# Performance work log

Hardware: AMD Instinct MI355X
Metric: run time of the kernel (lower is better)

The kernel has to match this reference:

```python
import jax, jax.numpy as jnp
import numpy as np

HID = 64   # RNN_HID_SIZE
FEAT = 9   # feature dim, hard-coded in module
T = 36     # SEQ_LEN


def setup_inputs() -> dict:
    key = jax.random.key(0)
    ks = jax.random.split(key, 20)
    B = 16384

    def u(k, shape, stdv):
        return jax.random.uniform(k, shape, jnp.float32, -stdv, stdv)

    s_h = 1.0 / np.sqrt(HID)    # stdv for layers with 64 rows / fan-in 64
    s_f = 1.0 / np.sqrt(FEAT)   # stdv 1/3 for feature-sized layers
    s_c = 1.0 / np.sqrt(2 * FEAT)  # weight_combine: Linear(18, 9)

    inp = {
        "values": jax.random.normal(ks[0], (B, T, FEAT), jnp.float32),
        "masks": (jax.random.uniform(ks[1], (B, T, FEAT)) < 0.8).astype(jnp.float32),
        "deltas": jax.random.uniform(ks[2], (B, T, FEAT), jnp.float32, 0.0, 5.0),
        # TemporalDecay h: W [64, 9], stdv = 1/sqrt(64)
        "W_gh": u(ks[3], (HID, FEAT), s_h), "b_gh": u(ks[4], (HID,), s_h),
        # TemporalDecay x (diag): W [9, 9], stdv = 1/sqrt(9)
        "W_gx": u(ks[5], (FEAT, FEAT), s_f), "b_gx": u(ks[6], (FEAT,), s_f),
        # hist_reg: Linear(64, 9)
        "W_hist": u(ks[7], (FEAT, HID), s_h), "b_hist": u(ks[8], (FEAT,), s_h),
        "W_feat": u(ks[9], (FEAT, FEAT), s_f), "b_feat": u(ks[10], (FEAT,), s_f),
        # weight_combine: Linear(18, 9)
        "W_comb": u(ks[11], (FEAT, 2 * FEAT), s_c), "b_comb": u(ks[12], (FEAT,), s_c),
        # LSTMCell(18, 64): gates order i, f, g, o
        "W_ih": u(ks[13], (4 * HID, 2 * FEAT), s_h), "W_hh": u(ks[14], (4 * HID, HID), s_h),
        "b_ih": u(ks[15], (4 * HID,), s_h), "b_hh": u(ks[16], (4 * HID,), s_h),
    }
    return inp


def reference(values, masks, deltas, W_gh, b_gh, W_gx, b_gx, W_hist, b_hist,
              W_feat, b_feat, W_comb, b_comb, W_ih, W_hh, b_ih, b_hh):
    B = values.shape[0]
    dt = values.dtype
    eye = jnp.eye(FEAT, dtype=dt)
    Wgx_diag = W_gx * eye            # TemporalDecay diag mask
    Wfeat_off = W_feat * (1.0 - eye)

    # time-major for scan: [T, B, F]
    xs = (jnp.swapaxes(values, 0, 1), jnp.swapaxes(masks, 0, 1), jnp.swapaxes(deltas, 0, 1))

    def step(carry, xt):
        h, c, loss = carry
        x, m, d = xt
        gamma_h = jnp.exp(-jax.nn.relu(d @ W_gh.T + b_gh))   # [B, 64]
        gamma_x = jnp.exp(-jax.nn.relu(d @ Wgx_diag.T + b_gx))  # [B, 9]
        h = h * gamma_h
        x_h = h @ W_hist.T + b_hist
        denom = jnp.sum(m) + 1e-5
        x_c = m * x + (1.0 - m) * x_h
        z_h = x_c @ Wfeat_off.T + b_feat
        alpha = jnp.concatenate([gamma_x, m], axis=1) @ W_comb.T + b_comb
        c_h = alpha * z_h + (1.0 - alpha) * x_h
        loss = loss + (jnp.sum(jnp.abs(x - x_h) * m)
                       + jnp.sum(jnp.abs(x - z_h) * m)
                       + jnp.sum(jnp.abs(x - c_h) * m)) / denom
        c_c = m * x + (1.0 - m) * c_h
        inp = jnp.concatenate([c_c, m], axis=1)              # [B, 18]
        gates = inp @ W_ih.T + b_ih + h @ W_hh.T + b_hh      # [B, 256]
        i, f, g, o = jnp.split(gates, 4, axis=1)
        c = jax.nn.sigmoid(f) * c + jax.nn.sigmoid(i) * jnp.tanh(g)
        h = jax.nn.sigmoid(o) * jnp.tanh(c)
        return (h, c, loss), c_c

    init = (jnp.zeros((B, HID), dt), jnp.zeros((B, HID), dt), jnp.zeros((), dt))
    (_, _, loss), imps = jax.lax.scan(step, init, xs)
    imputations = jnp.swapaxes(imps, 0, 1)  # [B, T, F]
    return loss / T, imputations
```

## Files before the change

kernel.cpp:

```cpp
#include <hip/hip_runtime.h>

typedef _Float16 hh;
typedef _Float16 h2  __attribute__((ext_vector_type(2)));
typedef _Float16 v4h __attribute__((ext_vector_type(4)));
typedef _Float16 v8h __attribute__((ext_vector_type(8)));
typedef float v4f    __attribute__((ext_vector_type(4)));
typedef unsigned short u16;

#define T_STEPS 36
#define FEAT 9
#define HID 64
#define BT 32
#define SIN_STR 232
#define PK_STR 40

__device__ __forceinline__ float fast_exp2(float x) {
#if __has_builtin(__builtin_amdgcn_exp2f)
  return __builtin_amdgcn_exp2f(x);
#else
  return exp2f(x);
#endif
}
__device__ __forceinline__ float fast_rcp(float x) {
#if __has_builtin(__builtin_amdgcn_rcpf)
  return __builtin_amdgcn_rcpf(x);
#else
  return 1.f / x;
#endif
}
__device__ __forceinline__ float sigmoid_fast(float x) {
  return fast_rcp(1.f + fast_exp2(x * -1.442695041f));
}
__device__ __forceinline__ float tanh_fast(float x) {
  return 1.f - 2.f * fast_rcp(1.f + fast_exp2(x * 2.885390082f));
}
__device__ __forceinline__ float fdot2(h2 a, h2 b, float c) {
#if __has_builtin(__builtin_amdgcn_fdot2)
  return __builtin_amdgcn_fdot2(a, b, c, false);
#else
  return c + (float)a[0] * (float)b[0] + (float)a[1] * (float)b[1];
#endif
}
__device__ __forceinline__ h2 mkh2(hh a, hh b) { h2 r; r[0] = a; r[1] = b; return r; }
__device__ __forceinline__ v4f mfma16(v8h a, v8h b, v4f c) {
  return __builtin_amdgcn_mfma_f32_16x16x32_f16(a, b, c, 0, 0, 0);
}

__global__ void zero_ws(float* __restrict__ ws, float* __restrict__ out) {
  int tid = threadIdx.x;
  if (tid < T_STEPS) ws[tid] = 0.f;
  if (tid == 0) out[0] = 0.f;
}

__global__ __launch_bounds__(256) void denom_kernel(const float* __restrict__ masks,
                                                    float* __restrict__ ws) {
  __shared__ float red[T_STEPS];
  const int tid = threadIdx.x;
  if (tid < T_STEPS) red[tid] = 0.f;
  __syncthreads();
  const int idx = blockIdx.x * 256 + tid;
  const int t0 = (idx % 9) * 4;
  const float4* p = (const float4*)masks + (size_t)idx * 9;
  float acc[4] = {0.f, 0.f, 0.f, 0.f};
#pragma unroll
  for (int c = 0; c < 9; ++c) {
    float4 v = p[c];
    acc[(4 * c) / 9]     += v.x;
    acc[(4 * c + 1) / 9] += v.y;
    acc[(4 * c + 2) / 9] += v.z;
    acc[(4 * c + 3) / 9] += v.w;
  }
#pragma unroll
  for (int j = 0; j < 4; ++j) atomicAdd(&red[t0 + j], acc[j]);
  __syncthreads();
  if (tid < T_STEPS) atomicAdd(&ws[tid], red[tid]);
}

#define BARX() asm volatile("s_waitcnt lgkmcnt(0)\n\ts_barrier" ::: "memory")

#define RITS_STEP(t, pxC,pmC,pdC,pxCb,pmCb,pdCb, pxN,pmN,pdN,pxNb,pmNb,pdNb)   \
  {                                                                            \
    const float inv_den = fast_rcp(denom[(t)] + 1e-5f);                        \
    const int pb = ((t) & 1) * 96;                                             \
         \
    v4f gacc[2];                                                               \
    {                                                                          \
      const int sel = ((t) + 1) & 1;                                           \
      const int awin = 176 + sel * 24;                                         \
      _Pragma("unroll")                                                        \
      for (int mt = 0; mt < 2; ++mt) {                                         \
        v8h a_ = *(const v8h*)&sIn[(mt * 16 + nlo) * SIN_STR + awin + q * 8];  \
        v4f z4 = {0.f, 0.f, 0.f, 0.f};                                         \
        gacc[mt] = sel ? mfma16(a_, bGamB, z4) : mfma16(a_, bGamA, z4);        \
      }                                                                        \
    }                                                                          \
       \
    {                                                                          \
      v4f xacc = {0.f, 0.f, 0.f, 0.f};                                         \
      _Pragma("unroll")                                                        \
      for (int kt = 0; kt < 3; ++kt) {                                         \
        v8h a_ = *(const v8h*)&sIn[(mtw * 16 + nlo) * SIN_STR + pb +           \
                                   kt * 32 + q * 8];                           \
        xacc = mfma16(a_, bH[kt], xacc);                                       \
      }                                                                        \
         \
      if ((q >> 1) == (wid & 1) && nlo < 9) {                                  \
        _Pragma("unroll")                                                      \
        for (int r = 0; r < 4; ++r)                                            \
          sPk[(mtw * 16 + q * 4 + r) * PK_STR + 18 + nlo] = (hh)xacc[r];       \
      }                                                                        \
    }                                                                          \
           \
    asm volatile("s_waitcnt lgkmcnt(0)" ::: "memory");                         \
                 \
    {                                                                          \
      const int pk = eP * PK_STR;                                              \
      float x_f  = (float)sPk[pk + fqw];                                       \
      float m_f  = (float)sPk[pk + 9 + fqw];                                   \
      float xh_f = (float)sPk[pk + 18 + fqw];                                  \
      v8h r0 = *(const v8h*)&sPk[pk];                                          \
      v8h r1 = *(const v8h*)&sPk[pk + 8];                                      \
      v8h r2 = *(const v8h*)&sPk[pk + 16];                                     \
      v8h r3 = *(const v8h*)&sPk[pk + 24];                                     \
      v4h r4 = *(const v4h*)&sPk[pk + 32];                                     \
      hh xxh[9] = {r0[0],r0[1],r0[2],r0[3],r0[4],r0[5],r0[6],r0[7],r1[0]};     \
      hh mmh[9] = {r1[1],r1[2],r1[3],r1[4],r1[5],r1[6],r1[7],r2[0],r2[1]};     \
      hh xhh[9] = {r2[2],r2[3],r2[4],r2[5],r2[6],r2[7],r3[0],r3[1],r3[2]};     \
      hh gxh[9] = {r3[3],r3[4],r3[5],r3[6],r3[7],r4[0],r4[1],r4[2],r4[3]};     \
      hh xch[10];                                                              \
      _Pragma("unroll")                                                        \
      for (int f = 0; f < 9; ++f) {                                            \
        u16 mb = __builtin_bit_cast(u16, mmh[f]);                              \
        xch[f] = mb ? xxh[f] : xhh[f];                                         \
      }                                                                        \
      xch[9] = (hh)0.f;                                                        \
      h2 xc2[5] = {mkh2(xch[0],xch[1]), mkh2(xch[2],xch[3]),                   \
                   mkh2(xch[4],xch[5]), mkh2(xch[6],xch[7]),                   \
                   mkh2(xch[8],xch[9])};                                       \
      h2 g2[9]  = {mkh2(gxh[0],gxh[1]), mkh2(gxh[2],gxh[3]),                   \
                   mkh2(gxh[4],gxh[5]), mkh2(gxh[6],gxh[7]),                   \
                   mkh2(gxh[8],mmh[0]), mkh2(mmh[1],mmh[2]),                   \
                   mkh2(mmh[3],mmh[4]), mkh2(mmh[5],mmh[6]),                   \
                   mkh2(mmh[7],mmh[8])};                                       \
                        \
      float z1a = bf1, z1b = 0.f;                                              \
      z1a = fdot2(wf1[0], xc2[0], z1a); z1b = fdot2(wf1[1], xc2[1], z1b);      \
      z1a = fdot2(wf1[2], xc2[2], z1a); z1b = fdot2(wf1[3], xc2[3], z1b);      \
      z1a = fdot2(wf1[4], xc2[4], z1a);                                        \
      float z1 = z1a + z1b;                                                    \
      float a1a = bc1v, a1b = 0.f, a1c = 0.f;                                  \
      a1a = fdot2(wc1[0], g2[0], a1a); a1b = fdot2(wc1[1], g2[1], a1b);        \
      a1c = fdot2(wc1[2], g2[2], a1c); a1a = fdot2(wc1[3], g2[3], a1a);        \
      a1b = fdot2(wc1[4], g2[4], a1b); a1c = fdot2(wc1[5], g2[5], a1c);        \
      a1a = fdot2(wc1[6], g2[6], a1a); a1b = fdot2(wc1[7], g2[7], a1b);        \
      a1c = fdot2(wc1[8], g2[8], a1c);                                         \
      float a1 = (a1a + a1b) + a1c;                                            \
      float ch1 = xh_f + a1 * (z1 - xh_f);                                     \
      bool obs1 = (m_f != 0.f);                                                \
      float cc1 = obs1 ? x_f : ch1;                                            \
      float lterm = obs1 ? (fabsf(x_f - xh_f) + fabsf(x_f - z1) +              \
                            fabsf(x_f - ch1)) : 0.f;                           \
      sIn[eP * SIN_STR + pb + fqw] = (hh)cc1;                                  \
      sIn[eP * SIN_STR + pb + 9 + fqw] = (hh)m_f;                              \
      out[1 + (size_t)(b0 + eP) * (T_STEPS * FEAT) + (t) * FEAT + fqw] = cc1;  \
      if (fqw == 7) {                                                          \
        float z2a = bf2, z2b = 0.f;                                            \
        z2a = fdot2(wf2[0], xc2[0], z2a); z2b = fdot2(wf2[1], xc2[1], z2b);    \
        z2a = fdot2(wf2[2], xc2[2], z2a); z2b = fdot2(wf2[3], xc2[3], z2b);    \
        z2a = fdot2(wf2[4], xc2[4], z2a);                                      \
        float z2 = z2a + z2b;                                                  \
        float a2a = bc2v, a2b = 0.f, a2c = 0.f;                                \
        a2a = fdot2(wc2[0], g2[0], a2a); a2b = fdot2(wc2[1], g2[1], a2b);      \
        a2c = fdot2(wc2[2], g2[2], a2c); a2a = fdot2(wc2[3], g2[3], a2a);      \
        a2b = fdot2(wc2[4], g2[4], a2b); a2c = fdot2(wc2[5], g2[5], a2c);      \
        a2a = fdot2(wc2[6], g2[6], a2a); a2b = fdot2(wc2[7], g2[7], a2b);      \
        a2c = fdot2(wc2[8], g2[8], a2c);                                       \
        float a2 = (a2a + a2b) + a2c;                                          \
        float x8 = (float)xxh[8], m8 = (float)mmh[8], xh8 = (float)xhh[8];     \
        float ch2 = xh8 + a2 * (z2 - xh8);                                     \
        bool obs2 = (m8 != 0.f);                                               \
        float cc2 = obs2 ? x8 : ch2;                                           \
        lterm += obs2 ? (fabsf(x8 - xh8) + fabsf(x8 - z2) +                    \
                         fabsf(x8 - ch2)) : 0.f;                               \
        sIn[eP * SIN_STR + pb + 8] = (hh)cc2;                                  \
        sIn[eP * SIN_STR + pb + 17] = mmh[8];                                  \
        out[1 + (size_t)(b0 + eP) * (T_STEPS * FEAT) + (t) * FEAT + 8] = cc2;  \
      }                                                                        \
      loss_acc += lterm * inv_den;                                             \
    }                                                                          \
    BARX();                                                                    \
      \
    {                                                                          \
      const bool ldN = ((t) + 2 < T_STEPS);                                    \
      const bool ldD = ((t) + 3 < T_STEPS);                                    \
      if (ldN) {                                                               \
        size_t offn = (size_t)(b0 + e1) * (T_STEPS * FEAT) +                   \
                      ((t) + 2) * FEAT + f1;                                   \
        pxN = values[offn]; pmN = masks[offn];                                 \
        if (tid < 32) {                                                        \
          size_t offn2 = (size_t)(b0 + e2g) * (T_STEPS * FEAT) +               \
                         ((t) + 2) * FEAT + f2g;                               \
          pxNb = values[offn2]; pmNb = masks[offn2];                           \
        }                                                                      \
      }                                                                        \
      if (ldD) {                                                               \
        size_t offd = (size_t)(b0 + e1) * (T_STEPS * FEAT) +                   \
                      ((t) + 3) * FEAT + f1;                                   \
        pdN = deltas[offd];                                                    \
        if (tid < 32) {                                                        \
          size_t offd2 = (size_t)(b0 + e2g) * (T_STEPS * FEAT) +               \
                         ((t) + 3) * FEAT + f2g;                               \
          pdNb = deltas[offd2];                                                \
        }                                                                      \
      }                                                                        \
      const int pub = (((t) + 1) & 1) * 96;                                    \
      v8h af[2][3];                                                            \
      _Pragma("unroll")                                                        \
      for (int mt = 0; mt < 2; ++mt)                                           \
        _Pragma("unroll")                                                      \
        for (int kt = 0; kt < 3; ++kt)                                         \
          af[mt][kt] = *(const v8h*)&sIn[(mt * 16 + nlo) * SIN_STR + pb +      \
                                         kt * 32 + q * 8];                     \
      v4f acc[2][4];                                                           \
      _Pragma("unroll")                                                        \
      for (int mt = 0; mt < 2; ++mt)                                           \
        _Pragma("unroll")                                                      \
        for (int p = 0; p < 4; ++p)                                            \
          acc[mt][p] = (v4f){0.f, 0.f, 0.f, 0.f};                              \
      _Pragma("unroll")                                                        \
      for (int mt = 0; mt < 2; ++mt)                                           \
        _Pragma("unroll")                                                      \
        for (int p = 0; p < 4; ++p)                                            \
          _Pragma("unroll")                                                    \
          for (int kt = 0; kt < 3; ++kt)                                       \
            acc[mt][p] = mfma16(af[mt][kt], bG[p][kt], acc[mt][p]);            \
      _Pragma("unroll")                                                        \
      for (int mt = 0; mt < 2; ++mt) {                                         \
        _Pragma("unroll")                                                      \
        for (int r = 0; r < 4; ++r) {                                          \
          float ig = sigmoid_fast(acc[mt][0][r]);                              \
          float fg = sigmoid_fast(acc[mt][1][r]);                              \
          float gg = tanh_fast(acc[mt][2][r]);                                 \
          float og = sigmoid_fast(acc[mt][3][r]);                              \
          float cn = fg * c_s[mt * 4 + r] + ig * gg;                           \
          c_s[mt * 4 + r] = cn;                                                \
          float hn = og * tanh_fast(cn);                                       \
          float gam = fast_exp2(fmaxf(gacc[mt][r], 0.f) * -1.442695041f);      \
          sIn[(mt * 16 + q * 4 + r) * SIN_STR + pub + 18 + j_col] =            \
              (hh)(hn * gam);                                                  \
        }                                                                      \
      }                                                                        \
      if ((t) + 1 < T_STEPS) {                                                 \
        sPk[e1 * PK_STR + f1] = (hh)pxC;                                       \
        sPk[e1 * PK_STR + 9 + f1] = (hh)pmC;                                   \
        sPk[e1 * PK_STR + 27 + f1] =                                           \
            (hh)fast_exp2(fmaxf(dH * wgx1 + bgx1, 0.f) * -1.442695041f);       \
        if (tid < 32) {                                                        \
          sPk[e2g * PK_STR + f2g] = (hh)pxCb;                                  \
          sPk[e2g * PK_STR + 9 + f2g] = (hh)pmCb;                              \
          sPk[e2g * PK_STR + 27 + f2g] =                                       \
              (hh)fast_exp2(fmaxf(dHb * wgx2 + bgx2, 0.f) * -1.442695041f);    \
        }                                                                      \
      }                                                                        \
      if ((t) + 2 < T_STEPS) {                                                 \
        const int sb = 192 + ((t) & 1) * 10;                                   \
        sIn[e1 * SIN_STR + sb + f1] = (hh)pdC;                                 \
        if (tid < 32) sIn[e2g * SIN_STR + sb + f2g] = (hh)pdCb;                \
      }                                                                        \
      dH = pdC; dHb = pdCb;                                                    \
    }                                                                          \
    BARX();                                                                    \
  }

__global__ __launch_bounds__(256, 2) void rits_kernel(
    const float* __restrict__ values, const float* __restrict__ masks,
    const float* __restrict__ deltas,
    const float* __restrict__ W_gh, const float* __restrict__ b_gh,
    const float* __restrict__ W_gx, const float* __restrict__ b_gx,
    const float* __restrict__ W_hist, const float* __restrict__ b_hist,
    const float* __restrict__ W_feat, const float* __restrict__ b_feat,
    const float* __restrict__ W_comb, const float* __restrict__ b_comb,
    const float* __restrict__ W_ih, const float* __restrict__ W_hh,
    const float* __restrict__ b_ih, const float* __restrict__ b_hh,
    const float* __restrict__ denom, float* __restrict__ out) {

  __shared__ __align__(16) hh sIn[BT * SIN_STR];
  __shared__ __align__(16) hh sPk[BT * PK_STR];
  __shared__ float sRed[256];

  const int tid = threadIdx.x;
  const int lane = tid & 63;
  const int wid = tid >> 6;
  const int q = lane >> 4;
  const int nlo = lane & 15;
  const int b0 = blockIdx.x * BT;
  const int j_col = 16 * wid + nlo;
  const int mtw = wid >> 1;

  v8h bG[4][3];
#pragma unroll
  for (int p = 0; p < 4; ++p)
#pragma unroll
    for (int kt = 0; kt < 3; ++kt) {
      int n = 64 * p + j_col;
      v8h r;
#pragma unroll
      for (int jj = 0; jj < 8; ++jj) {
        int k = kt * 32 + q * 8 + jj;
        float v = 0.f;
        if (k < 18)       v = W_ih[n * 18 + k];
        else if (k < 82)  v = W_hh[n * 64 + (k - 18)];
        else if (k == 82) v = b_ih[n] + b_hh[n];
        r[jj] = (hh)v;
      }
      bG[p][kt] = r;
    }
  v8h bH[3];
#pragma unroll
  for (int kt = 0; kt < 3; ++kt) {
    v8h r;
#pragma unroll
    for (int jj = 0; jj < 8; ++jj) {
      int k = kt * 32 + q * 8 + jj;
      float v = 0.f;
      if (nlo < 9) {
        if (k >= 18 && k < 82) v = W_hist[nlo * 64 + (k - 18)];
        else if (k == 82)      v = b_hist[nlo];
      }
      r[jj] = (hh)v;
    }
    bH[kt] = r;
  }
  v8h bGamA, bGamB;
  {
    int n = j_col;
    v8h ra, rb;
#pragma unroll
    for (int jj = 0; jj < 8; ++jj) {
      int k = q * 8 + jj;
      float va = 0.f, vb = 0.f;
      if (k == 2) va = b_gh[n];
      else if (k >= 16 && k < 25) va = W_gh[n * 9 + (k - 16)];
      if (k >= 2 && k < 11) vb = W_gh[n * 9 + (k - 2)];
      else if (k == 12) vb = b_gh[n];
      ra[jj] = (hh)va; rb[jj] = (hh)vb;
    }
    bGamA = ra; bGamB = rb;
  }

  const int eP = tid >> 3, fqw = tid & 7;
  h2 wf1[5], wf2[5], wc1[9], wc2[9];
  float bf1 = b_feat[fqw], bf2 = b_feat[8];
  float bc1v = b_comb[fqw], bc2v = b_comb[8];
#pragma unroll
  for (int j = 0; j < 5; ++j) {
    int i0 = 2 * j, i1 = 2 * j + 1;
    hh a0 = (hh)((i0 == fqw) ? 0.f : W_feat[fqw * 9 + i0]);
    hh a1 = (hh)((i1 < 9) ? ((i1 == fqw) ? 0.f : W_feat[fqw * 9 + i1]) : 0.f);
    wf1[j] = mkh2(a0, a1);
    hh c0 = (hh)((i0 == 8) ? 0.f : W_feat[8 * 9 + i0]);
    hh c1 = (hh)((i1 < 9) ? W_feat[8 * 9 + i1] : 0.f);
    wf2[j] = mkh2(c0, c1);
  }
#pragma unroll
  for (int j = 0; j < 9; ++j) {
    wc1[j] = mkh2((hh)W_comb[fqw * 18 + 2 * j], (hh)W_comb[fqw * 18 + 2 * j + 1]);
    wc2[j] = mkh2((hh)W_comb[8 * 18 + 2 * j], (hh)W_comb[8 * 18 + 2 * j + 1]);
  }

  const int e1 = tid / 9, f1 = tid - 9 * e1;
  const int e2g = (tid + 256) / 9, f2g = (tid + 256) - 9 * e2g;
  const float wgx1 = W_gx[f1 * 9 + f1], bgx1 = b_gx[f1];
  float wgx2 = 0.f, bgx2 = 0.f;
  if (tid < 32) { wgx2 = W_gx[f2g * 9 + f2g]; bgx2 = b_gx[f2g]; }

  for (int i = tid; i < BT * SIN_STR; i += 256) sIn[i] = (hh)0.f;
  __syncthreads();
  if (tid < BT) {
    sIn[tid * SIN_STR + 82] = (hh)1.f;
    sIn[tid * SIN_STR + 178] = (hh)1.f;
    sIn[tid * SIN_STR + 212] = (hh)1.f;
  }
  float pA_x = 0.f, pA_m = 0.f, pA_d = 0.f, pA_xb = 0.f, pA_mb = 0.f, pA_db = 0.f;
  float pB_x = 0.f, pB_m = 0.f, pB_d = 0.f, pB_xb = 0.f, pB_mb = 0.f, pB_db = 0.f;
  float dH = 0.f, dHb = 0.f;
  {
    size_t off = (size_t)(b0 + e1) * (T_STEPS * FEAT) + f1;
    float d0 = deltas[off];
    sPk[e1 * PK_STR + f1] = (hh)values[off];
    sPk[e1 * PK_STR + 9 + f1] = (hh)masks[off];
    sPk[e1 * PK_STR + 27 + f1] =
        (hh)fast_exp2(fmaxf(d0 * wgx1 + bgx1, 0.f) * -1.442695041f);
    float d1 = deltas[off + FEAT];
    dH = d1;
    sIn[e1 * SIN_STR + 202 + f1] = (hh)d1;
    pA_x = values[off + FEAT]; pA_m = masks[off + FEAT];
    pA_d = deltas[off + 2 * FEAT];
    if (tid < 32) {
      size_t off2 = (size_t)(b0 + e2g) * (T_STEPS * FEAT) + f2g;
      float d0b = deltas[off2];
      sPk[e2g * PK_STR + f2g] = (hh)values[off2];
      sPk[e2g * PK_STR + 9 + f2g] = (hh)masks[off2];
      sPk[e2g * PK_STR + 27 + f2g] =
          (hh)fast_exp2(fmaxf(d0b * wgx2 + bgx2, 0.f) * -1.442695041f);
      float d1b = deltas[off2 + FEAT];
      dHb = d1b;
      sIn[e2g * SIN_STR + 202 + f2g] = (hh)d1b;
      pA_xb = values[off2 + FEAT]; pA_mb = masks[off2 + FEAT];
      pA_db = deltas[off2 + 2 * FEAT];
    }
  }
  __syncthreads();

  float c_s[8];
#pragma unroll
  for (int i = 0; i < 8; ++i) c_s[i] = 0.f;
  float loss_acc = 0.f;

  for (int t = 0; t < T_STEPS; t += 2) {
    RITS_STEP(t,     pA_x, pA_m, pA_d, pA_xb, pA_mb, pA_db,
                     pB_x, pB_m, pB_d, pB_xb, pB_mb, pB_db);
    RITS_STEP(t + 1, pB_x, pB_m, pB_d, pB_xb, pB_mb, pB_db,
                     pA_x, pA_m, pA_d, pA_xb, pA_mb, pA_db);
  }

  sRed[tid] = loss_acc;
  __syncthreads();
  for (int k = 128; k > 0; k >>= 1) {
    if (tid < k) sRed[tid] += sRed[tid + k];
    __syncthreads();
  }
  if (tid == 0) atomicAdd(out, sRed[0] * (1.f / (float)T_STEPS));
}

extern "C" void kernel_launch(void* const* d_in, const int* in_sizes, int n_in,
                              void* d_out, int out_size, void* d_ws, size_t ws_size,
                              hipStream_t stream) {
  const float* values = (const float*)d_in[0];
  const float* masks  = (const float*)d_in[1];
  const float* deltas = (const float*)d_in[2];
  const float* W_gh   = (const float*)d_in[3];
  const float* b_gh   = (const float*)d_in[4];
  const float* W_gx   = (const float*)d_in[5];
  const float* b_gx   = (const float*)d_in[6];
  const float* W_hist = (const float*)d_in[7];
  const float* b_hist = (const float*)d_in[8];
  const float* W_feat = (const float*)d_in[9];
  const float* b_feat = (const float*)d_in[10];
  const float* W_comb = (const float*)d_in[11];
  const float* b_comb = (const float*)d_in[12];
  const float* W_ih   = (const float*)d_in[13];
  const float* W_hh   = (const float*)d_in[14];
  const float* b_ih   = (const float*)d_in[15];
  const float* b_hh   = (const float*)d_in[16];

  float* out = (float*)d_out;
  float* ws  = (float*)d_ws;
  int B = in_sizes[0] / (T_STEPS * FEAT);

  zero_ws<<<1, 64, 0, stream>>>(ws, out);
  denom_kernel<<<(B * 9) / 256, 256, 0, stream>>>(masks, ws);
  rits_kernel<<<B / BT, 256, 0, stream>>>(values, masks, deltas,
                                          W_gh, b_gh, W_gx, b_gx,
                                          W_hist, b_hist, W_feat, b_feat,
                                          W_comb, b_comb, W_ih, W_hh,
                                          b_ih, b_hh, ws, out);
}
```

Measured before the change: 245.4 us.

## Interleave two independent batch tiles per block to halve barriers per step

Each block now processes two 32-row batch tiles in lockstep, with separate shared buffers, cell states and prefetch registers per tile. The phases of both tiles are interleaved inside one step, so each pair of barriers covers twice the work and the independent instruction streams can hide each other's latency. The grid halves and launch bounds drop to one block per SM-equivalent, trading occupancy and register headroom for more instruction-level parallelism within a block.

```diff
diff --git a/kernel.cpp b/kernel.cpp
--- a/kernel.cpp
+++ b/kernel.cpp
@@ -11,6 +11,7 @@
 #define FEAT 9
 #define HID 64
 #define BT 32
+#define NT 2
 #define SIN_STR 232
 #define PK_STR 40
 
@@ -78,51 +79,48 @@
 
 #define BARX() asm volatile("s_waitcnt lgkmcnt(0)\n\ts_barrier" ::: "memory")
 
-#define RITS_STEP(t, pxC,pmC,pdC,pxCb,pmCb,pdCb, pxN,pmN,pdN,pxNb,pmNb,pdNb)   \
+
+#define TILE_GXH(t, TI)                                                        \
   {                                                                            \
-    const float inv_den = fast_rcp(denom[(t)] + 1e-5f);                        \
     const int pb = ((t) & 1) * 96;                                             \
-         \
-    v4f gacc[2];                                                               \
     {                                                                          \
       const int sel = ((t) + 1) & 1;                                           \
       const int awin = 176 + sel * 24;                                         \
       _Pragma("unroll")                                                        \
       for (int mt = 0; mt < 2; ++mt) {                                         \
-        v8h a_ = *(const v8h*)&sIn[(mt * 16 + nlo) * SIN_STR + awin + q * 8];  \
+        v8h a_ = *(const v8h*)&sIn##TI[(mt * 16 + nlo) * SIN_STR + awin + q * 8]; \
         v4f z4 = {0.f, 0.f, 0.f, 0.f};                                         \
-        gacc[mt] = sel ? mfma16(a_, bGamB, z4) : mfma16(a_, bGamA, z4);        \
+        gacc##TI[mt] = sel ? mfma16(a_, bGamB, z4) : mfma16(a_, bGamA, z4);    \
       }                                                                        \
     }                                                                          \
-       \
     {                                                                          \
       v4f xacc = {0.f, 0.f, 0.f, 0.f};                                         \
       _Pragma("unroll")                                                        \
       for (int kt = 0; kt < 3; ++kt) {                                         \
-        v8h a_ = *(const v8h*)&sIn[(mtw * 16 + nlo) * SIN_STR + pb +           \
-                                   kt * 32 + q * 8];                           \
+        v8h a_ = *(const v8h*)&sIn##TI[(mtw * 16 + nlo) * SIN_STR + pb +       \
+                                       kt * 32 + q * 8];                       \
         xacc = mfma16(a_, bH[kt], xacc);                                       \
       }                                                                        \
-         \
       if ((q >> 1) == (wid & 1) && nlo < 9) {                                  \
         _Pragma("unroll")                                                      \
         for (int r = 0; r < 4; ++r)                                            \
-          sPk[(mtw * 16 + q * 4 + r) * PK_STR + 18 + nlo] = (hh)xacc[r];       \
+          sPk##TI[(mtw * 16 + q * 4 + r) * PK_STR + 18 + nlo] = (hh)xacc[r];   \
       }                                                                        \
     }                                                                          \
-           \
-    asm volatile("s_waitcnt lgkmcnt(0)" ::: "memory");                         \
-                 \
+  }
+
+#define TILE_P2(t, TI)                                                         \
     {                                                                          \
+      const int pb = ((t) & 1) * 96;                                           \
       const int pk = eP * PK_STR;                                              \
-      float x_f  = (float)sPk[pk + fqw];                                       \
-      float m_f  = (float)sPk[pk + 9 + fqw];                                   \
-      float xh_f = (float)sPk[pk + 18 + fqw];                                  \
-      v8h r0 = *(const v8h*)&sPk[pk];                                          \
-      v8h r1 = *(const v8h*)&sPk[pk + 8];                                      \
-      v8h r2 = *(const v8h*)&sPk[pk + 16];                                     \
-      v8h r3 = *(const v8h*)&sPk[pk + 24];                                     \
-      v4h r4 = *(const v4h*)&sPk[pk + 32];                                     \
+      float x_f  = (float)sPk##TI[pk + fqw];                                   \
+      float m_f  = (float)sPk##TI[pk + 9 + fqw];                               \
+      float xh_f = (float)sPk##TI[pk + 18 + fqw];                              \
+      v8h r0 = *(const v8h*)&sPk##TI[pk];                                      \
+      v8h r1 = *(const v8h*)&sPk##TI[pk + 8];                                  \
+      v8h r2 = *(const v8h*)&sPk##TI[pk + 16];                                 \
+      v8h r3 = *(const v8h*)&sPk##TI[pk + 24];                                 \
+      v4h r4 = *(const v4h*)&sPk##TI[pk + 32];                                 \
       hh xxh[9] = {r0[0],r0[1],r0[2],r0[3],r0[4],r0[5],r0[6],r0[7],r1[0]};     \
       hh mmh[9] = {r1[1],r1[2],r1[3],r1[4],r1[5],r1[6],r1[7],r2[0],r2[1]};     \
       hh xhh[9] = {r2[2],r2[3],r2[4],r2[5],r2[6],r2[7],r3[0],r3[1],r3[2]};     \
@@ -142,7 +140,6 @@
                    mkh2(gxh[8],mmh[0]), mkh2(mmh[1],mmh[2]),                   \
                    mkh2(mmh[3],mmh[4]), mkh2(mmh[5],mmh[6]),                   \
                    mkh2(mmh[7],mmh[8])};                                       \
-                        \
       float z1a = bf1, z1b = 0.f;                                              \
       z1a = fdot2(wf1[0], xc2[0], z1a); z1b = fdot2(wf1[1], xc2[1], z1b);      \
       z1a = fdot2(wf1[2], xc2[2], z1a); z1b = fdot2(wf1[3], xc2[3], z1b);      \
@@ -160,9 +157,10 @@
       float cc1 = obs1 ? x_f : ch1;                                            \
       float lterm = obs1 ? (fabsf(x_f - xh_f) + fabsf(x_f - z1) +              \
                             fabsf(x_f - ch1)) : 0.f;                           \
-      sIn[eP * SIN_STR + pb + fqw] = (hh)cc1;                                  \
-      sIn[eP * SIN_STR + pb + 9 + fqw] = (hh)m_f;                              \
-      out[1 + (size_t)(b0 + eP) * (T_STEPS * FEAT) + (t) * FEAT + fqw] = cc1;  \
+      sIn##TI[eP * SIN_STR + pb + fqw] = (hh)cc1;                              \
+      sIn##TI[eP * SIN_STR + pb + 9 + fqw] = (hh)m_f;                          \
+      out[1 + (size_t)(b0T##TI + eP) * (T_STEPS * FEAT) + (t) * FEAT + fqw] =  \
+          cc1;                                                                 \
       if (fqw == 7) {                                                          \
         float z2a = bf2, z2b = 0.f;                                            \
         z2a = fdot2(wf2[0], xc2[0], z2a); z2b = fdot2(wf2[1], xc2[1], z2b);    \
@@ -182,45 +180,47 @@
         float cc2 = obs2 ? x8 : ch2;                                           \
         lterm += obs2 ? (fabsf(x8 - xh8) + fabsf(x8 - z2) +                    \
                          fabsf(x8 - ch2)) : 0.f;                               \
-        sIn[eP * SIN_STR + pb + 8] = (hh)cc2;                                  \
-        sIn[eP * SIN_STR + pb + 17] = mmh[8];                                  \
-        out[1 + (size_t)(b0 + eP) * (T_STEPS * FEAT) + (t) * FEAT + 8] = cc2;  \
+        sIn##TI[eP * SIN_STR + pb + 8] = (hh)cc2;                              \
+        sIn##TI[eP * SIN_STR + pb + 17] = mmh[8];                              \
+        out[1 + (size_t)(b0T##TI + eP) * (T_STEPS * FEAT) + (t) * FEAT + 8] =  \
+            cc2;                                                               \
       }                                                                        \
       loss_acc += lterm * inv_den;                                             \
-    }                                                                          \
-    BARX();                                                                    \
-      \
+    }
+
+#define TILE_B(t, TI, CUR, NXT)                                                \
     {                                                                          \
       const bool ldN = ((t) + 2 < T_STEPS);                                    \
       const bool ldD = ((t) + 3 < T_STEPS);                                    \
       if (ldN) {                                                               \
-        size_t offn = (size_t)(b0 + e1) * (T_STEPS * FEAT) +                   \
+        size_t offn = (size_t)(b0T##TI + e1) * (T_STEPS * FEAT) +              \
                       ((t) + 2) * FEAT + f1;                                   \
-        pxN = values[offn]; pmN = masks[offn];                                 \
+        p##TI##NXT##_x = values[offn]; p##TI##NXT##_m = masks[offn];           \
         if (tid < 32) {                                                        \
-          size_t offn2 = (size_t)(b0 + e2g) * (T_STEPS * FEAT) +               \
+          size_t offn2 = (size_t)(b0T##TI + e2g) * (T_STEPS * FEAT) +          \
                          ((t) + 2) * FEAT + f2g;                               \
-          pxNb = values[offn2]; pmNb = masks[offn2];                           \
+          p##TI##NXT##_xb = values[offn2]; p##TI##NXT##_mb = masks[offn2];     \
         }                                                                      \
       }                                                                        \
       if (ldD) {                                                               \
-        size_t offd = (size_t)(b0 + e1) * (T_STEPS * FEAT) +                   \
+        size_t offd = (size_t)(b0T##TI + e1) * (T_STEPS * FEAT) +              \
                       ((t) + 3) * FEAT + f1;                                   \
-        pdN = deltas[offd];                                                    \
+        p##TI##NXT##_d = deltas[offd];                                         \
         if (tid < 32) {                                                        \
-          size_t offd2 = (size_t)(b0 + e2g) * (T_STEPS * FEAT) +               \
+          size_t offd2 = (size_t)(b0T##TI + e2g) * (T_STEPS * FEAT) +          \
                          ((t) + 3) * FEAT + f2g;                               \
-          pdNb = deltas[offd2];                                                \
+          p##TI##NXT##_db = deltas[offd2];                                     \
         }                                                                      \
       }                                                                        \
+      const int pb = ((t) & 1) * 96;                                           \
       const int pub = (((t) + 1) & 1) * 96;                                    \
       v8h af[2][3];                                                            \
       _Pragma("unroll")                                                        \
       for (int mt = 0; mt < 2; ++mt)                                           \
         _Pragma("unroll")                                                      \
         for (int kt = 0; kt < 3; ++kt)                                         \
-          af[mt][kt] = *(const v8h*)&sIn[(mt * 16 + nlo) * SIN_STR + pb +      \
-                                         kt * 32 + q * 8];                     \
+          af[mt][kt] = *(const v8h*)&sIn##TI[(mt * 16 + nlo) * SIN_STR + pb +  \
+                                             kt * 32 + q * 8];                 \
       v4f acc[2][4];                                                           \
       _Pragma("unroll")                                                        \
       for (int mt = 0; mt < 2; ++mt)                                           \
@@ -242,37 +242,49 @@
           float fg = sigmoid_fast(acc[mt][1][r]);                              \
           float gg = tanh_fast(acc[mt][2][r]);                                 \
           float og = sigmoid_fast(acc[mt][3][r]);                              \
-          float cn = fg * c_s[mt * 4 + r] + ig * gg;                           \
-          c_s[mt * 4 + r] = cn;                                                \
+          float cn = fg * cs##TI[mt * 4 + r] + ig * gg;                        \
+          cs##TI[mt * 4 + r] = cn;                                             \
           float hn = og * tanh_fast(cn);                                       \
-          float gam = fast_exp2(fmaxf(gacc[mt][r], 0.f) * -1.442695041f);      \
-          sIn[(mt * 16 + q * 4 + r) * SIN_STR + pub + 18 + j_col] =            \
+          float gam = fast_exp2(fmaxf(gacc##TI[mt][r], 0.f) * -1.442695041f);  \
+          sIn##TI[(mt * 16 + q * 4 + r) * SIN_STR + pub + 18 + j_col] =        \
               (hh)(hn * gam);                                                  \
         }                                                                      \
       }                                                                        \
       if ((t) + 1 < T_STEPS) {                                                 \
-        sPk[e1 * PK_STR + f1] = (hh)pxC;                                       \
-        sPk[e1 * PK_STR + 9 + f1] = (hh)pmC;                                   \
-        sPk[e1 * PK_STR + 27 + f1] =                                           \
-            (hh)fast_exp2(fmaxf(dH * wgx1 + bgx1, 0.f) * -1.442695041f);       \
+        sPk##TI[e1 * PK_STR + f1] = (hh)p##TI##CUR##_x;                        \
+        sPk##TI[e1 * PK_STR + 9 + f1] = (hh)p##TI##CUR##_m;                    \
+        sPk##TI[e1 * PK_STR + 27 + f1] =                                       \
+            (hh)fast_exp2(fmaxf(dH##TI * wgx1 + bgx1, 0.f) * -1.442695041f);   \
         if (tid < 32) {                                                        \
-          sPk[e2g * PK_STR + f2g] = (hh)pxCb;                                  \
-          sPk[e2g * PK_STR + 9 + f2g] = (hh)pmCb;                              \
-          sPk[e2g * PK_STR + 27 + f2g] =                                       \
-              (hh)fast_exp2(fmaxf(dHb * wgx2 + bgx2, 0.f) * -1.442695041f);    \
+          sPk##TI[e2g * PK_STR + f2g] = (hh)p##TI##CUR##_xb;                   \
+          sPk##TI[e2g * PK_STR + 9 + f2g] = (hh)p##TI##CUR##_mb;               \
+          sPk##TI[e2g * PK_STR + 27 + f2g] =                                   \
+              (hh)fast_exp2(fmaxf(dHb##TI * wgx2 + bgx2, 0.f) * -1.442695041f);\
         }                                                                      \
       }                                                                        \
       if ((t) + 2 < T_STEPS) {                                                 \
         const int sb = 192 + ((t) & 1) * 10;                                   \
-        sIn[e1 * SIN_STR + sb + f1] = (hh)pdC;                                 \
-        if (tid < 32) sIn[e2g * SIN_STR + sb + f2g] = (hh)pdCb;                \
-      }                                                                        \
-      dH = pdC; dHb = pdCb;                                                    \
-    }                                                                          \
+        sIn##TI[e1 * SIN_STR + sb + f1] = (hh)p##TI##CUR##_d;                  \
+        if (tid < 32) sIn##TI[e2g * SIN_STR + sb + f2g] = (hh)p##TI##CUR##_db; \
+      }                                                                        \
+      dH##TI = p##TI##CUR##_d; dHb##TI = p##TI##CUR##_db;                      \
+    }
+
+#define FULL_STEP(t, CUR, NXT)                                                 \
+  {                                                                            \
+    const float inv_den = fast_rcp(denom[(t)] + 1e-5f);                        \
+    TILE_GXH(t, 0)                                                             \
+    TILE_GXH(t, 1)                                                             \
+    asm volatile("s_waitcnt lgkmcnt(0)" ::: "memory");                         \
+    TILE_P2(t, 0)                                                              \
+    TILE_P2(t, 1)                                                              \
     BARX();                                                                    \
-  }
-
-__global__ __launch_bounds__(256, 2) void rits_kernel(
+    TILE_B(t, 0, CUR, NXT)                                                     \
+    TILE_B(t, 1, CUR, NXT)                                                     \
+    BARX();                                                                    \
+  }
+
+__global__ __launch_bounds__(256, 1) void rits_kernel(
     const float* __restrict__ values, const float* __restrict__ masks,
     const float* __restrict__ deltas,
     const float* __restrict__ W_gh, const float* __restrict__ b_gh,
@@ -284,16 +296,21 @@
     const float* __restrict__ b_ih, const float* __restrict__ b_hh,
     const float* __restrict__ denom, float* __restrict__ out) {
 
-  __shared__ __align__(16) hh sIn[BT * SIN_STR];
-  __shared__ __align__(16) hh sPk[BT * PK_STR];
+  __shared__ __align__(16) hh sInAll[NT * BT * SIN_STR];
+  __shared__ __align__(16) hh sPkAll[NT * BT * PK_STR];
   __shared__ float sRed[256];
+  hh* sIn0 = sInAll;
+  hh* sIn1 = sInAll + BT * SIN_STR;
+  hh* sPk0 = sPkAll;
+  hh* sPk1 = sPkAll + BT * PK_STR;
 
   const int tid = threadIdx.x;
   const int lane = tid & 63;
   const int wid = tid >> 6;
   const int q = lane >> 4;
   const int nlo = lane & 15;
-  const int b0 = blockIdx.x * BT;
+  const int b0T0 = blockIdx.x * (BT * NT);
+  const int b0T1 = b0T0 + BT;
   const int j_col = 16 * wid + nlo;
   const int mtw = wid >> 1;
 
@@ -374,54 +391,81 @@
   float wgx2 = 0.f, bgx2 = 0.f;
   if (tid < 32) { wgx2 = W_gx[f2g * 9 + f2g]; bgx2 = b_gx[f2g]; }
 
-  for (int i = tid; i < BT * SIN_STR; i += 256) sIn[i] = (hh)0.f;
+  for (int i = tid; i < NT * BT * SIN_STR; i += 256) sInAll[i] = (hh)0.f;
   __syncthreads();
-  if (tid < BT) {
-    sIn[tid * SIN_STR + 82] = (hh)1.f;
-    sIn[tid * SIN_STR + 178] = (hh)1.f;
-    sIn[tid * SIN_STR + 212] = (hh)1.f;
-  }
-  float pA_x = 0.f, pA_m = 0.f, pA_d = 0.f, pA_xb = 0.f, pA_mb = 0.f, pA_db = 0.f;
-  float pB_x = 0.f, pB_m = 0.f, pB_d = 0.f, pB_xb = 0.f, pB_mb = 0.f, pB_db = 0.f;
-  float dH = 0.f, dHb = 0.f;
+  if (tid < NT * BT) {
+    hh* S = (tid < BT) ? sIn0 : sIn1;
+    int rr = (tid < BT) ? tid : tid - BT;
+    S[rr * SIN_STR + 82] = (hh)1.f;
+    S[rr * SIN_STR + 178] = (hh)1.f;
+    S[rr * SIN_STR + 212] = (hh)1.f;
+  }
+  float p0A_x = 0.f, p0A_m = 0.f, p0A_d = 0.f, p0A_xb = 0.f, p0A_mb = 0.f, p0A_db = 0.f;
+  float p0B_x = 0.f, p0B_m = 0.f, p0B_d = 0.f, p0B_xb = 0.f, p0B_mb = 0.f, p0B_db = 0.f;
+  float p1A_x = 0.f, p1A_m = 0.f, p1A_d = 0.f, p1A_xb = 0.f, p1A_mb = 0.f, p1A_db = 0.f;
+  float p1B_x = 0.f, p1B_m = 0.f, p1B_d = 0.f, p1B_xb = 0.f, p1B_mb = 0.f, p1B_db = 0.f;
+  float dH0 = 0.f, dHb0 = 0.f, dH1 = 0.f, dHb1 = 0.f;
   {
-    size_t off = (size_t)(b0 + e1) * (T_STEPS * FEAT) + f1;
+    size_t off = (size_t)(b0T0 + e1) * (T_STEPS * FEAT) + f1;
     float d0 = deltas[off];
-    sPk[e1 * PK_STR + f1] = (hh)values[off];
-    sPk[e1 * PK_STR + 9 + f1] = (hh)masks[off];
-    sPk[e1 * PK_STR + 27 + f1] =
+    sPk0[e1 * PK_STR + f1] = (hh)values[off];
+    sPk0[e1 * PK_STR + 9 + f1] = (hh)masks[off];
+    sPk0[e1 * PK_STR + 27 + f1] =
         (hh)fast_exp2(fmaxf(d0 * wgx1 + bgx1, 0.f) * -1.442695041f);
     float d1 = deltas[off + FEAT];
-    dH = d1;
-    sIn[e1 * SIN_STR + 202 + f1] = (hh)d1;
-    pA_x = values[off + FEAT]; pA_m = masks[off + FEAT];
-    pA_d = deltas[off + 2 * FEAT];
+    dH0 = d1;
+    sIn0[e1 * SIN_STR + 202 + f1] = (hh)d1;
+    p0A_x = values[off + FEAT]; p0A_m = masks[off + FEAT];
+    p0A_d = deltas[off + 2 * FEAT];
     if (tid < 32) {
-      size_t off2 = (size_t)(b0 + e2g) * (T_STEPS * FEAT) + f2g;
+      size_t off2 = (size_t)(b0T0 + e2g) * (T_STEPS * FEAT) + f2g;
       float d0b = deltas[off2];
-      sPk[e2g * PK_STR + f2g] = (hh)values[off2];
-      sPk[e2g * PK_STR + 9 + f2g] = (hh)masks[off2];
-      sPk[e2g * PK_STR + 27 + f2g] =
+      sPk0[e2g * PK_STR + f2g] = (hh)values[off2];
+      sPk0[e2g * PK_STR + 9 + f2g] = (hh)masks[off2];
+      sPk0[e2g * PK_STR + 27 + f2g] =
           (hh)fast_exp2(fmaxf(d0b * wgx2 + bgx2, 0.f) * -1.442695041f);
       float d1b = deltas[off2 + FEAT];
-      dHb = d1b;
-      sIn[e2g * SIN_STR + 202 + f2g] = (hh)d1b;
-      pA_xb = values[off2 + FEAT]; pA_mb = masks[off2 + FEAT];
-      pA_db = deltas[off2 + 2 * FEAT];
+      dHb0 = d1b;
+      sIn0[e2g * SIN_STR + 202 + f2g] = (hh)d1b;
+      p0A_xb = values[off2 + FEAT]; p0A_mb = masks[off2 + FEAT];
+      p0A_db = deltas[off2 + 2 * FEAT];
+    }
+    size_t offT = (size_t)(b0T1 + e1) * (T_STEPS * FEAT) + f1;
+    float d0T = deltas[offT];
+    sPk1[e1 * PK_STR + f1] = (hh)values[offT];
+    sPk1[e1 * PK_STR + 9 + f1] = (hh)masks[offT];
+    sPk1[e1 * PK_STR + 27 + f1] =
+        (hh)fast_exp2(fmaxf(d0T * wgx1 + bgx1, 0.f) * -1.442695041f);
+    float d1T = deltas[offT + FEAT];
+    dH1 = d1T;
+    sIn1[e1 * SIN_STR + 202 + f1] = (hh)d1T;
+    p1A_x = values[offT + FEAT]; p1A_m = masks[offT + FEAT];
+    p1A_d = deltas[offT + 2 * FEAT];
+    if (tid < 32) {
+      size_t off2T = (size_t)(b0T1 + e2g) * (T_STEPS * FEAT) + f2g;
+      float d0bT = deltas[off2T];
+      sPk1[e2g * PK_STR + f2g] = (hh)values[off2T];
+      sPk1[e2g * PK_STR + 9 + f2g] = (hh)masks[off2T];
+      sPk1[e2g * PK_STR + 27 + f2g] =
+          (hh)fast_exp2(fmaxf(d0bT * wgx2 + bgx2, 0.f) * -1.442695041f);
+      float d1bT = deltas[off2T + FEAT];
+      dHb1 = d1bT;
+      sIn1[e2g * SIN_STR + 202 + f2g] = (hh)d1bT;
+      p1A_xb = values[off2T + FEAT]; p1A_mb = masks[off2T + FEAT];
+      p1A_db = deltas[off2T + 2 * FEAT];
     }
   }
   __syncthreads();
 
-  float c_s[8];
-#pragma unroll
-  for (int i = 0; i < 8; ++i) c_s[i] = 0.f;
+  float cs0[8], cs1[8];
+#pragma unroll
+  for (int i = 0; i < 8; ++i) { cs0[i] = 0.f; cs1[i] = 0.f; }
+  v4f gacc0[2], gacc1[2];
   float loss_acc = 0.f;
 
   for (int t = 0; t < T_STEPS; t += 2) {
-    RITS_STEP(t,     pA_x, pA_m, pA_d, pA_xb, pA_mb, pA_db,
-                     pB_x, pB_m, pB_d, pB_xb, pB_mb, pB_db);
-    RITS_STEP(t + 1, pB_x, pB_m, pB_d, pB_xb, pB_mb, pB_db,
-                     pA_x, pA_m, pA_d, pA_xb, pA_mb, pA_db);
+    FULL_STEP(t, A, B)
+    FULL_STEP(t + 1, B, A)
   }
 
   sRed[tid] = loss_acc;
@@ -460,9 +504,9 @@
 
   zero_ws<<<1, 64, 0, stream>>>(ws, out);
   denom_kernel<<<(B * 9) / 256, 256, 0, stream>>>(masks, ws);
-  rits_kernel<<<B / BT, 256, 0, stream>>>(values, masks, deltas,
-                                          W_gh, b_gh, W_gx, b_gx,
-                                          W_hist, b_hist, W_feat, b_feat,
-                                          W_comb, b_comb, W_ih, W_hh,
-                                          b_ih, b_hh, ws, out);
-}
+  rits_kernel<<<B / (BT * NT), 256, 0, stream>>>(values, masks, deltas,
+                                                 W_gh, b_gh, W_gx, b_gx,
+                                                 W_hist, b_hist, W_feat, b_feat,
+                                                 W_comb, b_comb, W_ih, W_hh,
+                                                 b_ih, b_hh, ws, out);
+}
```

New measurement: 263.5 us. 1.07x slower.
